# Kernel tuning notes

Hardware: AMD Instinct MI355X
Metric: run time of the kernel (lower is better)

Reference implementation:

```python
import jax, jax.numpy as jnp
import numpy as np
import math

B, T, V, D, H, L = 32, 512, 16, 256, 4, 2

def _ln(x, g, b, eps=1e-5):
    m = jnp.mean(x, -1, keepdims=True)
    v = jnp.mean((x - m) ** 2, -1, keepdims=True)
    return (x - m) * jax.lax.rsqrt(v + eps) * g + b

def _grn(x, w1, b1, w2, b2, g, bn, sw=None, sb=None):
    h = jax.nn.elu(x @ w1 + b1)
    h = h @ w2 + b2
    h1, h2 = jnp.split(h, 2, axis=-1)
    h = h1 * jax.nn.sigmoid(h2)
    skip = x if sw is None else x @ sw + sb
    return _ln(h + skip, g, bn)

def setup_inputs():
    ks = iter(jax.random.split(jax.random.key(0), 64))
    s = 0.02
    def w(*shape):
        return jax.random.normal(next(ks), shape, jnp.float32) * s
    return dict(
        x=jax.random.normal(next(ks), (B, T, V), jnp.float32),
        emb_w=w(V, D), emb_b=w(V, D),
        vg_fc1_w=w(V, D, D), vg_fc1_b=w(V, D), vg_fc2_w=w(V, D, 2 * D), vg_fc2_b=w(V, 2 * D),
        vg_ln_g=jnp.ones((V, D), jnp.float32), vg_ln_b=jnp.zeros((V, D), jnp.float32),
        sel_fc1_w=w(V * D, D), sel_fc1_b=w(D), sel_fc2_w=w(D, 2 * V), sel_fc2_b=w(2 * V),
        sel_skip_w=w(V * D, V), sel_skip_b=w(V),
        sel_ln_g=jnp.ones((V,), jnp.float32), sel_ln_b=jnp.zeros((V,), jnp.float32),
        lstm_wih=w(L, 4 * D, D), lstm_whh=w(L, 4 * D, D), lstm_bih=w(L, 4 * D), lstm_bhh=w(L, 4 * D),
        pl_fc1_w=w(D, D), pl_fc1_b=w(D), pl_fc2_w=w(D, 2 * D), pl_fc2_b=w(2 * D),
        pl_ln_g=jnp.ones((D,), jnp.float32), pl_ln_b=jnp.zeros((D,), jnp.float32),
        attn_in_w=w(3 * D, D), attn_in_b=w(3 * D), attn_out_w=w(D, D), attn_out_b=w(D),
        attn_ln_g=jnp.ones((D,), jnp.float32), attn_ln_b=jnp.zeros((D,), jnp.float32),
        pa_fc1_w=w(D, D), pa_fc1_b=w(D), pa_fc2_w=w(D, 2 * D), pa_fc2_b=w(2 * D),
        pa_ln_g=jnp.ones((D,), jnp.float32), pa_ln_b=jnp.zeros((D,), jnp.float32),
        fg_fc1_w=w(D, 4 * D), fg_fc1_b=w(4 * D), fg_fc2_w=w(4 * D, 2 * D), fg_fc2_b=w(2 * D),
        fg_ln_g=jnp.ones((D,), jnp.float32), fg_ln_b=jnp.zeros((D,), jnp.float32),
    )

def reference(x, emb_w, emb_b, vg_fc1_w, vg_fc1_b, vg_fc2_w, vg_fc2_b, vg_ln_g, vg_ln_b,
              sel_fc1_w, sel_fc1_b, sel_fc2_w, sel_fc2_b, sel_skip_w, sel_skip_b, sel_ln_g, sel_ln_b,
              lstm_wih, lstm_whh, lstm_bih, lstm_bhh,
              pl_fc1_w, pl_fc1_b, pl_fc2_w, pl_fc2_b, pl_ln_g, pl_ln_b,
              attn_in_w, attn_in_b, attn_out_w, attn_out_b, attn_ln_g, attn_ln_b,
              pa_fc1_w, pa_fc1_b, pa_fc2_w, pa_fc2_b, pa_ln_g, pa_ln_b,
              fg_fc1_w, fg_fc1_b, fg_fc2_w, fg_fc2_b, fg_ln_g, fg_ln_b):
    b, t, v = x.shape
    d = emb_w.shape[1]
    # per-feature Linear(1, d) fused into one broadcasted op: [B,T,V,D]
    embedded = x[..., None] * emb_w + emb_b
    # per-variable GRNs (no skip_fc since input==output), batched over V via einsum
    h = jax.nn.elu(jnp.einsum('btvd,vdh->btvh', embedded, vg_fc1_w) + vg_fc1_b)
    h = jnp.einsum('btvh,vho->btvo', h, vg_fc2_w) + vg_fc2_b
    h1, h2 = jnp.split(h, 2, axis=-1)
    var_out = _ln(h1 * jax.nn.sigmoid(h2) + embedded, vg_ln_g, vg_ln_b)  # [B,T,V,D]
    # selection GRN over flattened variables
    flat = embedded.reshape(b, t, v * d)
    sel = _grn(flat, sel_fc1_w, sel_fc1_b, sel_fc2_w, sel_fc2_b, sel_ln_g, sel_ln_b, sel_skip_w, sel_skip_b)
    weights = jax.nn.softmax(sel, axis=-1)  # [B,T,V]
    vsn_out = jnp.einsum('btvh,btv->bth', var_out, weights)  # [B,T,D]
    # stacked LSTM (torch gate order i,f,g,o); dropout inactive at eval
    h_seq = vsn_out
    for l in range(lstm_wih.shape[0]):
        xi = jnp.einsum('btd,gd->btg', h_seq, lstm_wih[l]) + lstm_bih[l] + lstm_bhh[l]
        whh = lstm_whh[l]
        def step(carry, xt):
            hp, cp = carry
            gates = xt + hp @ whh.T
            i, f, g, o = jnp.split(gates, 4, axis=-1)
            c = jax.nn.sigmoid(f) * cp + jax.nn.sigmoid(i) * jnp.tanh(g)
            hh = jax.nn.sigmoid(o) * jnp.tanh(c)
            return (hh, c), hh
        init = (jnp.zeros((b, d), x.dtype), jnp.zeros((b, d), x.dtype))
        _, hs = jax.lax.scan(step, init, jnp.swapaxes(xi, 0, 1))
        h_seq = jnp.swapaxes(hs, 0, 1)
    lstm_filtered = _grn(h_seq + vsn_out, pl_fc1_w, pl_fc1_b, pl_fc2_w, pl_fc2_b, pl_ln_g, pl_ln_b)
    # multihead self-attention
    qkv = lstm_filtered @ attn_in_w.T + attn_in_b
    q, k, vv = jnp.split(qkv, 3, axis=-1)
    hd = d // H
    def heads(z):
        return z.reshape(b, t, H, hd).transpose(0, 2, 1, 3)
    q, k, vv = heads(q), heads(k), heads(vv)
    scale = 1.0 / math.sqrt(hd)
    att = jax.nn.softmax(jnp.einsum('bhqd,bhkd->bhqk', q, k) * scale, axis=-1)
    o = jnp.einsum('bhqk,bhkd->bhqd', att, vv).transpose(0, 2, 1, 3).reshape(b, t, d)
    o = o @ attn_out_w.T + attn_out_b
    attn_out = _ln(o + lstm_filtered, attn_ln_g, attn_ln_b)
    attn_filtered = _grn(attn_out, pa_fc1_w, pa_fc1_b, pa_fc2_w, pa_fc2_b, pa_ln_g, pa_ln_b)
    out = _grn(attn_filtered, fg_fc1_w, fg_fc1_b, fg_fc2_w, fg_fc2_b, fg_ln_g, fg_ln_b)
    return out[:, -1, :], weights
```

## Files before the change

### kernel.cpp

```cpp
#include <hip/hip_runtime.h>
#include <hip/hip_bf16.h>
#include <hip/hip_fp8.h>
#include <math.h>


#define BT 16384
#define TT 512
#define BB 32
#define VV 16
#define DD 256

typedef unsigned short ushort;
typedef unsigned int uint;
typedef unsigned long ulong_;
typedef __attribute__((ext_vector_type(8))) short short8;
typedef __attribute__((ext_vector_type(8))) unsigned short ushort8v;
typedef __attribute__((ext_vector_type(4))) float floatx4;
typedef __attribute__((ext_vector_type(8))) int int8v;

#if __has_builtin(__builtin_amdgcn_cvt_pk_fp8_f32)
#define HW_FP8_CVT 1
#endif

__device__ __forceinline__ float sigmoidf_(float x) { return 1.f / (1.f + expf(-x)); }
__device__ __forceinline__ float eluf_(float x)     { return x > 0.f ? x : expm1f(x); }
__device__ __forceinline__ float fsig(float x) {
  return __builtin_amdgcn_rcpf(1.f + __expf(-x));
}
__device__ __forceinline__ float ftanh(float x) {
  float xc = fminf(fmaxf(x, -44.f), 44.f);
  float e = __expf(-2.f * xc);
  return (1.f - e) * __builtin_amdgcn_rcpf(1.f + e);
}
__device__ __forceinline__ ushort f2bf(float f) {
  unsigned int u = __float_as_uint(f);
  unsigned int r = u + 0x7fffu + ((u >> 16) & 1u);
  return (ushort)(r >> 16);
}
__device__ __forceinline__ float bf2f(ushort b) { return __uint_as_float(((unsigned int)b) << 16); }

__device__ __forceinline__ float2 bsum256x2(float a, float b, float* red8) {
  #pragma unroll
  for (int m = 32; m > 0; m >>= 1) { a += __shfl_xor(a, m, 64); b += __shfl_xor(b, m, 64); }
  int w = threadIdx.x >> 6;
  if ((threadIdx.x & 63) == 0) { red8[w * 2] = a; red8[w * 2 + 1] = b; }
  __syncthreads();
  float ra = red8[0] + red8[2] + red8[4] + red8[6];
  float rb = red8[1] + red8[3] + red8[5] + red8[7];
  __syncthreads();
  return make_float2(ra, rb);
}

__device__ __forceinline__ float block_sum256(float v, float* red) {
  int j = threadIdx.x;
  red[j] = v; __syncthreads();
  #pragma unroll
  for (int st = 128; st > 0; st >>= 1) {
    if (j < st) red[j] += red[j + st];
    __syncthreads();
  }
  float r = red[0];
  __syncthreads();
  return r;
}

__global__ void wtT_k(const float* __restrict__ src, ushort* __restrict__ dst,
                      int K, int N, long sStride, long dStride) {
  int b = blockIdx.z;
  src += (size_t)b * sStride; dst += (size_t)b * dStride;
  __shared__ float t[32][33];
  int k0 = blockIdx.y * 32, n0 = blockIdx.x * 32;
  int tx = threadIdx.x & 31, ty = threadIdx.x >> 5;
  #pragma unroll
  for (int i = 0; i < 32; i += 8) {
    int k = k0 + ty + i, n = n0 + tx;
    t[ty + i][tx] = (k < K && n < N) ? src[(size_t)k * N + n] : 0.f;
  }
  __syncthreads();
  #pragma unroll
  for (int i = 0; i < 32; i += 8) {
    int n = n0 + ty + i, k = k0 + tx;
    if (n < N && k < K) dst[(size_t)n * K + k] = f2bf(t[tx][ty + i]);
  }
}

__global__ void cvt_k(const float* __restrict__ src, ushort* __restrict__ dst, int n) {
  int i = blockIdx.x * 256 + threadIdx.x;
  if (i < n) dst[i] = f2bf(src[i]);
}

__global__ void whh_pack8_k(const float* __restrict__ whh, unsigned char* __restrict__ dst) {
  int gid = blockIdx.x * 256 + threadIdx.x;
  int layer = gid >> 13;
  int rem = gid & 8191;
  int lane = rem & 63;
  int f = (rem >> 6) & 15;
  int wave = rem >> 10;
  int kt2 = f & 1, ts = (f >> 1) & 1, g = f >> 2;
  int n = g * 256 + wave * 32 + ts * 16 + (lane & 15);
  int k0 = kt2 * 128 + (lane >> 4) * 32;
  const float* src = whh + (size_t)layer * 262144 + (size_t)n * 256 + k0;
  unsigned char* d = dst + (size_t)gid * 32;
  #pragma unroll
  for (int b = 0; b < 32; b++) {
    __hip_fp8_e4m3 q(src[b] * 64.f);
    d[b] = q.__x;
  }
}

template<int ADT, int ACT, int CDT>
__global__ __launch_bounds__(256) void mgemm_k(
    const void* __restrict__ Aall, int lda, long aStride,
    const ushort* __restrict__ Ball, long bStride,
    const float* __restrict__ biasAll, long biasStride,
    void* __restrict__ Call, int ldc, long cStride,
    int K, int Nvalid,
    const float* __restrict__ embw, const float* __restrict__ embb, int xbase) {
  int z = blockIdx.z;
  const ushort* B = Ball + (size_t)z * bStride;
  const float* bias = biasAll ? biasAll + (size_t)z * biasStride : nullptr;
  int m0 = blockIdx.y * 128, n0 = blockIdx.x * 128;
  __shared__ ushort As[128][40];
  __shared__ ushort Bs[128][40];
  int tid = threadIdx.x;
  int r = tid >> 1, half = tid & 1;
  int wave = tid >> 6, lane = tid & 63;
  int wm = (wave >> 1) * 64, wn = (wave & 1) * 64;
  int lm = lane & 15, lq = lane >> 4;
  floatx4 acc[4][4];
  #pragma unroll
  for (int i = 0; i < 4; i++)
    #pragma unroll
    for (int j = 0; j < 4; j++) acc[i][j] = (floatx4)0.f;

  for (int k0 = 0; k0 < K; k0 += 32) {
    int kk = k0 + half * 16;
    {
      int gm = m0 + r;
      ushort tmp[16];
      if (ADT == 0) {
        const float* Af = (const float*)Aall + (size_t)z * aStride + (size_t)gm * lda + kk;
        #pragma unroll
        for (int q = 0; q < 4; q++) {
          float4 f = ((const float4*)Af)[q];
          tmp[q * 4 + 0] = f2bf(f.x); tmp[q * 4 + 1] = f2bf(f.y);
          tmp[q * 4 + 2] = f2bf(f.z); tmp[q * 4 + 3] = f2bf(f.w);
        }
      } else if (ADT == 1) {
        const ushort* Ab = (const ushort*)Aall + (size_t)z * aStride + (size_t)gm * lda + kk;
        *(ushort8v*)&tmp[0] = *(const ushort8v*)(Ab);
        *(ushort8v*)&tmp[8] = *(const ushort8v*)(Ab + 8);
      } else if (ADT == 2) {
        const float* xp = (const float*)Aall;
        float xv = xp[(size_t)gm * lda + xbase + z + (kk >> 8)];
        const float4* ew = (const float4*)(embw + (size_t)z * 256 + kk);
        const float4* eb = (const float4*)(embb + (size_t)z * 256 + kk);
        #pragma unroll
        for (int q = 0; q < 4; q++) {
          float4 w4 = ew[q], b4 = eb[q];
          tmp[q * 4 + 0] = f2bf(xv * w4.x + b4.x); tmp[q * 4 + 1] = f2bf(xv * w4.y + b4.y);
          tmp[q * 4 + 2] = f2bf(xv * w4.z + b4.z); tmp[q * 4 + 3] = f2bf(xv * w4.w + b4.w);
        }
      } else {
        const float* A1 = (const float*)Aall + (size_t)z * aStride + (size_t)gm * lda + kk;
        const float* A2 = embw + (size_t)z * aStride + (size_t)gm * lda + kk;
        #pragma unroll
        for (int q = 0; q < 4; q++) {
          float4 f1 = ((const float4*)A1)[q];
          float4 f2 = ((const float4*)A2)[q];
          tmp[q * 4 + 0] = f2bf(f1.x + f2.x); tmp[q * 4 + 1] = f2bf(f1.y + f2.y);
          tmp[q * 4 + 2] = f2bf(f1.z + f2.z); tmp[q * 4 + 3] = f2bf(f1.w + f2.w);
        }
      }
      *(ushort8v*)&As[r][half * 16]     = *(ushort8v*)&tmp[0];
      *(ushort8v*)&As[r][half * 16 + 8] = *(ushort8v*)&tmp[8];
    }
    {
      int gn = n0 + r;
      ushort tmp[16];
      if (gn < Nvalid) {
        const ushort* Bp = B + (size_t)gn * K + kk;
        *(ushort8v*)&tmp[0] = *(const ushort8v*)(Bp);
        *(ushort8v*)&tmp[8] = *(const ushort8v*)(Bp + 8);
      } else {
        #pragma unroll
        for (int q = 0; q < 16; q++) tmp[q] = 0;
      }
      *(ushort8v*)&Bs[r][half * 16]     = *(ushort8v*)&tmp[0];
      *(ushort8v*)&Bs[r][half * 16 + 8] = *(ushort8v*)&tmp[8];
    }
    __syncthreads();
    short8 fa[4], fb[4];
    #pragma unroll
    for (int i = 0; i < 4; i++) fa[i] = *(const short8*)&As[wm + i * 16 + lm][lq * 8];
    #pragma unroll
    for (int j = 0; j < 4; j++) fb[j] = *(const short8*)&Bs[wn + j * 16 + lm][lq * 8];
    #pragma unroll
    for (int i = 0; i < 4; i++)
      #pragma unroll
      for (int j = 0; j < 4; j++)
        acc[i][j] = __builtin_amdgcn_mfma_f32_16x16x32_bf16(fa[i], fb[j], acc[i][j], 0, 0, 0);
    __syncthreads();
  }
  #pragma unroll
  for (int j = 0; j < 4; j++) {
    int gn = n0 + wn + j * 16 + lm;
    if (gn >= Nvalid) continue;
    float bv = bias ? bias[gn] : 0.f;
    #pragma unroll
    for (int i = 0; i < 4; i++) {
      #pragma unroll
      for (int rg = 0; rg < 4; rg++) {
        int gm = m0 + wm + i * 16 + lq * 4 + rg;
        float v = acc[i][j][rg] + bv;
        if (ACT == 1) v = eluf_(v);
        if (CDT == 0) ((float*)Call + (size_t)z * cStride)[(size_t)gm * ldc + gn] = v;
        else ((ushort*)Call + (size_t)z * cStride)[(size_t)gm * ldc + gn] = f2bf(v);
      }
    }
  }
}

__global__ void sel_finish_k(const float* __restrict__ selG, const float* __restrict__ selSkip,
                             const float* __restrict__ lng, const float* __restrict__ lnb,
                             float* __restrict__ wout, int M) {
  int m = blockIdx.x * 256 + threadIdx.x;
  if (m >= M) return;
  float s[16];
  float mean = 0.f;
  #pragma unroll
  for (int i = 0; i < 16; i++) {
    float h1 = selG[m * 32 + i], h2 = selG[m * 32 + 16 + i];
    float val = h1 * sigmoidf_(h2) + selSkip[m * 16 + i];
    s[i] = val; mean += val;
  }
  mean *= (1.f / 16.f);
  float var = 0.f;
  #pragma unroll
  for (int i = 0; i < 16; i++) { float d = s[i] - mean; var += d * d; }
  var *= (1.f / 16.f);
  float inv = rsqrtf(var + 1e-5f);
  float mx = -1e30f;
  #pragma unroll
  for (int i = 0; i < 16; i++) { s[i] = (s[i] - mean) * inv * lng[i] + lnb[i]; mx = fmaxf(mx, s[i]); }
  float sum = 0.f;
  #pragma unroll
  for (int i = 0; i < 16; i++) { s[i] = expf(s[i] - mx); sum += s[i]; }
  float isum = 1.f / sum;
  #pragma unroll
  for (int i = 0; i < 16; i++) wout[m * 16 + i] = s[i] * isum;
}

__global__ __launch_bounds__(256) void var_epi4_k(
    const ushort* __restrict__ G16,
    const float* __restrict__ x, int vbase,
    const float* __restrict__ embw, const float* __restrict__ embb,
    const float* __restrict__ lng, const float* __restrict__ lnb,
    const float* __restrict__ wts, float* __restrict__ vsn, int first) {
  int m = blockIdx.x, j = threadIdx.x;
  __shared__ float red8[8];
  float accv = 0.f;
  #pragma unroll
  for (int z = 0; z < 4; z++) {
    int v = vbase + z;
    const ushort* Gp = G16 + ((size_t)z * BT + m) * 512;
    float g1 = bf2f(Gp[j]), g2 = bf2f(Gp[256 + j]);
    float e = x[m * VV + v] * embw[z * 256 + j] + embb[z * 256 + j];
    float s = g1 * sigmoidf_(g2) + e;
    float2 r = bsum256x2(s, s * s, red8);
    float mean = r.x * (1.f / 256.f);
    float var = r.y * (1.f / 256.f) - mean * mean;
    float o = (s - mean) * rsqrtf(var + 1e-5f) * lng[z * 256 + j] + lnb[z * 256 + j];
    accv += wts[m * VV + v] * o;
  }
  size_t oi = (size_t)m * 256 + j;
  if (first) vsn[oi] = accv; else vsn[oi] += accv;
}

__global__ __launch_bounds__(256) void grn_epi_k(
    const ushort* __restrict__ G, const float* __restrict__ skipA,
    const float* __restrict__ skipB,
    const float* __restrict__ lng, const float* __restrict__ lnb,
    float* __restrict__ out) {
  int m = blockIdx.x, j = threadIdx.x;
  __shared__ float red8[8];
  float g1 = bf2f(G[(size_t)m * 512 + j]), g2 = bf2f(G[(size_t)m * 512 + 256 + j]);
  float sk = skipA[(size_t)m * 256 + j];
  if (skipB) sk += skipB[(size_t)m * 256 + j];
  float s = g1 * sigmoidf_(g2) + sk;
  float2 r = bsum256x2(s, s * s, red8);
  float mean = r.x * (1.f / 256.f);
  float var = r.y * (1.f / 256.f) - mean * mean;
  out[(size_t)m * 256 + j] = (s - mean) * rsqrtf(var + 1e-5f) * lng[j] + lnb[j];
}

__global__ void add2_k(const float* __restrict__ a, const float* __restrict__ b,
                       float* __restrict__ c, int n) {
  int i = blockIdx.x * 256 + threadIdx.x;
  if (i < n) c[i] = a[i] + b[i];
}

#define DESC (1.f / 1024.f)
#define H8S 272
__global__ __launch_bounds__(512, 2) void lstm_recur_k(
    const float* __restrict__ xi,
    const unsigned char* __restrict__ wpk,
    float* __restrict__ hout,
    int T) {
  int bb = blockIdx.x;
  int tid = threadIdx.x;
  int wave = tid >> 6, lane = tid & 63;
  int lm = lane & 15, lq = lane >> 4;
  __shared__ __align__(16) unsigned char h8[2][16 * H8S];
  for (int i = tid; i < 2 * 16 * H8S / 4; i += 512) ((uint*)h8)[i] = 0;

  int8v wr[16];
  {
    const int8v* wp = (const int8v*)wpk;
    #pragma unroll
    for (int f = 0; f < 16; f++) wr[f] = wp[(wave * 16 + f) * 64 + lane];
  }
  bool act = (lq == 0);
  int jj = wave * 32 + lm;
  const float* xg = xi + (size_t)bb * T * 1024;
  float xq[8], xn[8];
  if (act) {
    #pragma unroll
    for (int g = 0; g < 4; g++) {
      xq[2 * g]     = xg[g * 256 + jj];
      xq[2 * g + 1] = xg[g * 256 + jj + 16];
    }
  }
  float cst[2] = {0.f, 0.f};
  float hbf[2][8];
  int arow = lm * H8S + lq * 32;
  __syncthreads();

  for (int t = 0; t < T; t++) {
    int cur = t & 1, nxt = cur ^ 1;
    if (act && t + 1 < T) {
      const float* xp = xg + (size_t)(t + 1) * 1024;
      #pragma unroll
      for (int g = 0; g < 4; g++) {
        xn[2 * g]     = xp[g * 256 + jj];
        xn[2 * g + 1] = xp[g * 256 + jj + 16];
      }
    }
    int8v a[2];
    #pragma unroll
    for (int kt = 0; kt < 2; kt++)
      a[kt] = *(const int8v*)&h8[cur][arow + kt * 128];
    floatx4 acc[8];
    #pragma unroll
    for (int f = 0; f < 8; f++) acc[f] = (floatx4)0.f;
    #pragma unroll
    for (int kt = 0; kt < 2; kt++)
      #pragma unroll
      for (int f = 0; f < 8; f++)
        acc[f] = __builtin_amdgcn_mfma_scale_f32_16x16x128_f8f6f4(
            a[kt], wr[f * 2 + kt], acc[f], 0, 0, 0, 0x7f7f7f7f, 0, 0x7f7f7f7f);
    if (act) {
      int tb = t & 7;
      #pragma unroll
      for (int ts = 0; ts < 2; ts++) {
        float pi = acc[0 + ts][0] * DESC + xq[0 + ts];
        float pf = acc[2 + ts][0] * DESC + xq[2 + ts];
        float pg = acc[4 + ts][0] * DESC + xq[4 + ts];
        float po = acc[6 + ts][0] * DESC + xq[6 + ts];
        float c = fsig(pf) * cst[ts] + fsig(pi) * ftanh(pg);
        cst[ts] = c;
        hbf[ts][tb] = fsig(po) * ftanh(c);
      }
#ifdef HW_FP8_CVT
      int pk = __builtin_amdgcn_cvt_pk_fp8_f32(hbf[0][tb] * 16.f, hbf[1][tb] * 16.f, 0, false);
      h8[nxt][jj]      = (unsigned char)(pk & 0xff);
      h8[nxt][jj + 16] = (unsigned char)((pk >> 8) & 0xff);
#else
      __hip_fp8_e4m3 q0(hbf[0][tb] * 16.f), q1(hbf[1][tb] * 16.f);
      h8[nxt][jj]      = q0.__x;
      h8[nxt][jj + 16] = q1.__x;
#endif
      if (tb == 7) {
        #pragma unroll
        for (int q = 0; q < 8; q++) {
          size_t base = ((size_t)(bb * T + t - 7 + q)) * 256;
          hout[base + jj]      = hbf[0][q];
          hout[base + jj + 16] = hbf[1][q];
        }
      }
      #pragma unroll
      for (int g = 0; g < 8; g++) xq[g] = xn[g];
    }
    __syncthreads();
  }
}

__global__ __launch_bounds__(256) void attn_decode_k(const float* __restrict__ qkv,
                                                     float* __restrict__ o, int T) {
  int bh = blockIdx.x; int b = bh >> 2, h = bh & 3;
  int tid = threadIdx.x;
  __shared__ float q[64];
  __shared__ float p[512];
  __shared__ float red[256];
  if (tid < 64) q[tid] = qkv[((size_t)(b * T + T - 1)) * 768 + h * 64 + tid];
  __syncthreads();
  for (int t = tid; t < 512; t += 256) {
    const float* kv = qkv + ((size_t)(b * T + t)) * 768 + 256 + h * 64;
    float s = 0.f;
    #pragma unroll 16
    for (int d = 0; d < 64; d++) s += q[d] * kv[d];
    p[t] = s * 0.125f;
  }
  __syncthreads();
  red[tid] = fmaxf(p[tid], p[tid + 256]); __syncthreads();
  for (int st = 128; st > 0; st >>= 1) { if (tid < st) red[tid] = fmaxf(red[tid], red[tid + st]); __syncthreads(); }
  float mx = red[0]; __syncthreads();
  float e0 = expf(p[tid] - mx), e1 = expf(p[tid + 256] - mx);
  red[tid] = e0 + e1; __syncthreads();
  for (int st = 128; st > 0; st >>= 1) { if (tid < st) red[tid] += red[tid + st]; __syncthreads(); }
  float inv = 1.f / red[0];
  __syncthreads();
  p[tid] = e0; p[tid + 256] = e1;
  __syncthreads();
  int d = tid & 63, grp = tid >> 6;
  float acc = 0.f;
  for (int t = grp * 128; t < grp * 128 + 128; t++)
    acc += p[t] * qkv[((size_t)(b * T + t)) * 768 + 512 + h * 64 + d];
  red[tid] = acc; __syncthreads();
  if (grp == 0)
    o[(b * 4 + h) * 64 + d] = (red[tid] + red[tid + 64] + red[tid + 128] + red[tid + 192]) * inv;
}

__global__ __launch_bounds__(256) void attn_proj_ln_k(
    const float* __restrict__ attnO, const float* __restrict__ W, const float* __restrict__ bias,
    const float* __restrict__ lstmF, const float* __restrict__ lng, const float* __restrict__ lnb,
    float* __restrict__ out, int T) {
  int bb = blockIdx.x, j = threadIdx.x;
  __shared__ float a[256];
  __shared__ float red[256];
  a[j] = attnO[bb * 256 + j];
  __syncthreads();
  float acc = bias[j];
  const float* wr = W + (size_t)j * 256;
  #pragma unroll 8
  for (int k = 0; k < 256; k += 4) {
    float4 w4 = *(const float4*)(wr + k);
    acc += a[k] * w4.x + a[k + 1] * w4.y + a[k + 2] * w4.z + a[k + 3] * w4.w;
  }
  float s = acc + lstmF[((size_t)(bb * T + T - 1)) * 256 + j];
  float mean = block_sum256(s, red) * (1.f / 256.f);
  float d = s - mean;
  float var = block_sum256(d * d, red) * (1.f / 256.f);
  out[bb * 256 + j] = d * rsqrtf(var + 1e-5f) * lng[j] + lnb[j];
}

__global__ __launch_bounds__(256) void final_grns_k(
    const float* __restrict__ ain,
    const float* __restrict__ paw1, const float* __restrict__ pab1,
    const float* __restrict__ paw2, const float* __restrict__ pab2,
    const float* __restrict__ palg, const float* __restrict__ palb,
    const float* __restrict__ fgw1, const float* __restrict__ fgb1,
    const float* __restrict__ fgw2, const float* __restrict__ fgb2,
    const float* __restrict__ fglg, const float* __restrict__ fglb,
    float* __restrict__ out) {
  int bb = blockIdx.x, j = threadIdx.x;
  __shared__ float a[256];
  __shared__ float hbuf[1024];
  __shared__ float red[256];
  a[j] = ain[bb * 256 + j];
  __syncthreads();
  float acc = pab1[j];
  for (int k = 0; k < 256; k++) acc += a[k] * paw1[k * 256 + j];
  hbuf[j] = eluf_(acc);
  __syncthreads();
  float g1 = pab2[j], g2 = pab2[256 + j];
  for (int k = 0; k < 256; k++) { float hv = hbuf[k]; g1 += hv * paw2[k * 512 + j]; g2 += hv * paw2[k * 512 + 256 + j]; }
  float s = g1 * sigmoidf_(g2) + a[j];
  float mean = block_sum256(s, red) * (1.f / 256.f);
  float d = s - mean;
  float var = block_sum256(d * d, red) * (1.f / 256.f);
  float af = d * rsqrtf(var + 1e-5f) * palg[j] + palb[j];
  __syncthreads();
  a[j] = af;
  __syncthreads();
  float hh[4];
  #pragma unroll
  for (int q = 0; q < 4; q++) {
    int jj = j + q * 256;
    float ac = fgb1[jj];
    for (int k = 0; k < 256; k++) ac += a[k] * fgw1[k * 1024 + jj];
    hh[q] = eluf_(ac);
  }
  __syncthreads();
  #pragma unroll
  for (int q = 0; q < 4; q++) hbuf[j + q * 256] = hh[q];
  __syncthreads();
  float G1 = fgb2[j], G2 = fgb2[256 + j];
  for (int k = 0; k < 1024; k++) { float hv = hbuf[k]; G1 += hv * fgw2[k * 512 + j]; G2 += hv * fgw2[k * 512 + 256 + j]; }
  float s2 = G1 * sigmoidf_(G2) + a[j];
  mean = block_sum256(s2, red) * (1.f / 256.f);
  d = s2 - mean;
  var = block_sum256(d * d, red) * (1.f / 256.f);
  out[bb * 256 + j] = d * rsqrtf(var + 1e-5f) * fglg[j] + fglb[j];
}

extern "C" void kernel_launch(void* const* d_in, const int* in_sizes, int n_in,
                              void* d_out, int out_size, void* d_ws, size_t ws_size,
                              hipStream_t stream) {
  const float* x          = (const float*)d_in[0];
  const float* emb_w      = (const float*)d_in[1];
  const float* emb_b      = (const float*)d_in[2];
  const float* vg_fc1_w   = (const float*)d_in[3];
  const float* vg_fc1_b   = (const float*)d_in[4];
  const float* vg_fc2_w   = (const float*)d_in[5];
  const float* vg_fc2_b   = (const float*)d_in[6];
  const float* vg_ln_g    = (const float*)d_in[7];
  const float* vg_ln_b    = (const float*)d_in[8];
  const float* sel_fc1_w  = (const float*)d_in[9];
  const float* sel_fc1_b  = (const float*)d_in[10];
  const float* sel_fc2_w  = (const float*)d_in[11];
  const float* sel_fc2_b  = (const float*)d_in[12];
  const float* sel_skip_w = (const float*)d_in[13];
  const float* sel_skip_b = (const float*)d_in[14];
  const float* sel_ln_g   = (const float*)d_in[15];
  const float* sel_ln_b   = (const float*)d_in[16];
  const float* lstm_wih   = (const float*)d_in[17];
  const float* lstm_whh   = (const float*)d_in[18];
  const float* lstm_bih   = (const float*)d_in[19];
  const float* lstm_bhh   = (const float*)d_in[20];
  const float* pl_fc1_w   = (const float*)d_in[21];
  const float* pl_fc1_b   = (const float*)d_in[22];
  const float* pl_fc2_w   = (const float*)d_in[23];
  const float* pl_fc2_b   = (const float*)d_in[24];
  const float* pl_ln_g    = (const float*)d_in[25];
  const float* pl_ln_b    = (const float*)d_in[26];
  const float* attn_in_w  = (const float*)d_in[27];
  const float* attn_in_b  = (const float*)d_in[28];
  const float* attn_out_w = (const float*)d_in[29];
  const float* attn_out_b = (const float*)d_in[30];
  const float* attn_ln_g  = (const float*)d_in[31];
  const float* attn_ln_b  = (const float*)d_in[32];
  const float* pa_fc1_w   = (const float*)d_in[33];
  const float* pa_fc1_b   = (const float*)d_in[34];
  const float* pa_fc2_w   = (const float*)d_in[35];
  const float* pa_fc2_b   = (const float*)d_in[36];
  const float* pa_ln_g    = (const float*)d_in[37];
  const float* pa_ln_b    = (const float*)d_in[38];
  const float* fg_fc1_w   = (const float*)d_in[39];
  const float* fg_fc1_b   = (const float*)d_in[40];
  const float* fg_fc2_w   = (const float*)d_in[41];
  const float* fg_fc2_b   = (const float*)d_in[42];
  const float* fg_ln_g    = (const float*)d_in[43];
  const float* fg_ln_b    = (const float*)d_in[44];
  (void)in_sizes; (void)n_in; (void)out_size; (void)ws_size;

  float* out     = (float*)d_out;
  float* out_wts = out + BB * DD;

  char* p = (char*)d_ws;
  ushort* wt_sel_fc1  = (ushort*)p;                 p += 1048576 * 2;
  ushort* wt_sel_skip = (ushort*)p;                 p += 65536 * 2;
  ushort* wt_sel_fc2  = (ushort*)p;                 p += 8192 * 2;
  ushort* wt_var_fc1  = (ushort*)p;                 p += 1048576 * 2;
  ushort* wt_var_fc2  = (ushort*)p;                 p += 2097152 * 2;
  ushort* wt_wih      = (ushort*)p;                 p += 524288 * 2;
  unsigned char* wt_whh_pk8 = (unsigned char*)p;    p += 524288;
  ushort* wt_pl_fc1   = (ushort*)p;                 p += 65536 * 2;
  ushort* wt_pl_fc2   = (ushort*)p;                 p += 131072 * 2;
  ushort* wt_attn     = (ushort*)p;                 p += 196608 * 2;
  ushort* selH        = (ushort*)p;                 p += (size_t)BT * 256 * 2;
  float*  selSkip     = (float*)p;                  p += (size_t)BT * 16 * 4;
  float*  selG        = (float*)p;                  p += (size_t)BT * 32 * 4;
  float*  vsn         = (float*)p;                  p += (size_t)BT * 256 * 4;
  float*  hseq1       = (float*)p;                  p += (size_t)BT * 256 * 4;
  float*  hseq2       = (float*)p;                  p += (size_t)BT * 256 * 4;
  float*  cbias       = (float*)p;                  p += 4096 * 4;
  float*  attnO       = (float*)p;                  p += 8192 * 4;
  float*  attnLN      = (float*)p;                  p += 8192 * 4;
  char*   R           = p;
  ushort* bufA16 = (ushort*)R;
  ushort* bufG16 = (ushort*)(R + (((size_t)32) << 20));
  float*  xi     = (float*)R;
  ushort* plH    = (ushort*)(R + (((size_t)16) << 20));
  ushort* plG    = (ushort*)(R + (((size_t)24) << 20));
  float*  lstmF  = (float*)(R + (((size_t)48) << 20));
  float*  qkv    = (float*)R;

  dim3 blk(256);

  wtT_k<<<dim3(8, 128, 1),  blk, 0, stream>>>(sel_fc1_w,  wt_sel_fc1,  4096, 256, 0, 0);
  wtT_k<<<dim3(1, 128, 1),  blk, 0, stream>>>(sel_skip_w, wt_sel_skip, 4096, 16,  0, 0);
  wtT_k<<<dim3(1, 8, 1),    blk, 0, stream>>>(sel_fc2_w,  wt_sel_fc2,  256,  32,  0, 0);
  wtT_k<<<dim3(8, 8, 16),   blk, 0, stream>>>(vg_fc1_w,   wt_var_fc1,  256,  256, 65536, 65536);
  wtT_k<<<dim3(16, 8, 16),  blk, 0, stream>>>(vg_fc2_w,   wt_var_fc2,  256,  512, 131072, 131072);
  wtT_k<<<dim3(8, 8, 1),    blk, 0, stream>>>(pl_fc1_w,   wt_pl_fc1,   256,  256, 0, 0);
  wtT_k<<<dim3(16, 8, 1),   blk, 0, stream>>>(pl_fc2_w,   wt_pl_fc2,   256,  512, 0, 0);
  cvt_k<<<2048, blk, 0, stream>>>(lstm_wih,  wt_wih, 524288);
  whh_pack8_k<<<64, blk, 0, stream>>>(lstm_whh, wt_whh_pk8);
  cvt_k<<<768,  blk, 0, stream>>>(attn_in_w, wt_attn, 196608);
  add2_k<<<8, blk, 0, stream>>>(lstm_bih, lstm_bhh, cbias, 4096);

  mgemm_k<2,1,1><<<dim3(2, 128, 1), blk, 0, stream>>>(x, 16, 0, wt_sel_fc1, 0, sel_fc1_b, 0,
      selH, 256, 0, 4096, 256, emb_w, emb_b, 0);
  mgemm_k<2,0,0><<<dim3(1, 128, 1), blk, 0, stream>>>(x, 16, 0, wt_sel_skip, 0, sel_skip_b, 0,
      selSkip, 16, 0, 4096, 16, emb_w, emb_b, 0);
  mgemm_k<1,0,0><<<dim3(1, 128, 1), blk, 0, stream>>>(selH, 256, 0, wt_sel_fc2, 0, sel_fc2_b, 0,
      selG, 32, 0, 256, 32, nullptr, nullptr, 0);
  sel_finish_k<<<64, blk, 0, stream>>>(selG, selSkip, sel_ln_g, sel_ln_b, out_wts, BT);

  for (int g = 0; g < 4; g++) {
    mgemm_k<2,1,1><<<dim3(2, 128, 4), blk, 0, stream>>>(x, 16, 0,
        wt_var_fc1 + (size_t)g * 4 * 65536, 65536, vg_fc1_b + g * 1024, 256,
        bufA16, 256, (long)BT * 256, 256, 256, emb_w + g * 1024, emb_b + g * 1024, g * 4);
    mgemm_k<1,0,1><<<dim3(4, 128, 4), blk, 0, stream>>>(bufA16, 256, (long)BT * 256,
        wt_var_fc2 + (size_t)g * 4 * 131072, 131072, vg_fc2_b + g * 2048, 512,
        bufG16, 512, (long)BT * 512, 256, 512, nullptr, nullptr, 0);
    var_epi4_k<<<BT, blk, 0, stream>>>(bufG16, x, g * 4, emb_w + g * 1024, emb_b + g * 1024,
        vg_ln_g + g * 1024, vg_ln_b + g * 1024, out_wts, vsn, g == 0 ? 1 : 0);
  }

  mgemm_k<0,0,0><<<dim3(8, 128, 1), blk, 0, stream>>>(vsn, 256, 0, wt_wih, 0, cbias, 0,
      xi, 1024, 0, 256, 1024, nullptr, nullptr, 0);
  lstm_recur_k<<<32, 512, 0, stream>>>(xi, wt_whh_pk8, hseq1, TT);
  mgemm_k<0,0,0><<<dim3(8, 128, 1), blk, 0, stream>>>(hseq1, 256, 0, wt_wih + 1024 * 256, 0,
      cbias + 1024, 0, xi, 1024, 0, 256, 1024, nullptr, nullptr, 0);
  lstm_recur_k<<<32, 512, 0, stream>>>(xi, wt_whh_pk8 + 262144, hseq2, TT);

  mgemm_k<3,1,1><<<dim3(2, 128, 1), blk, 0, stream>>>(hseq2, 256, 0, wt_pl_fc1, 0, pl_fc1_b, 0,
      plH, 256, 0, 256, 256, vsn, nullptr, 0);
  mgemm_k<1,0,1><<<dim3(4, 128, 1), blk, 0, stream>>>(plH, 256, 0, wt_pl_fc2, 0, pl_fc2_b, 0,
      plG, 512, 0, 256, 512, nullptr, nullptr, 0);
  grn_epi_k<<<BT, blk, 0, stream>>>(plG, hseq2, vsn, pl_ln_g, pl_ln_b, lstmF);

  mgemm_k<0,0,0><<<dim3(6, 128, 1), blk, 0, stream>>>(lstmF, 256, 0, wt_attn, 0, attn_in_b, 0,
      qkv, 768, 0, 256, 768, nullptr, nullptr, 0);
  attn_decode_k<<<BB * 4, blk, 0, stream>>>(qkv, attnO, TT);
  attn_proj_ln_k<<<BB, blk, 0, stream>>>(attnO, attn_out_w, attn_out_b, lstmF,
                                         attn_ln_g, attn_ln_b, attnLN, TT);

  final_grns_k<<<BB, blk, 0, stream>>>(attnLN,
      pa_fc1_w, pa_fc1_b, pa_fc2_w, pa_fc2_b, pa_ln_g, pa_ln_b,
      fg_fc1_w, fg_fc1_b, fg_fc2_w, fg_fc2_b, fg_ln_g, fg_ln_b,
      out);
}
```

Baseline: 2.425 ms.

## Fold rank-1 embedding into first-layer weights, replacing K=4096 and K=256 GEMMs

Each embedded input is x*emb_w + emb_b, so the first linear layer of the selection GRN, its skip projection and each per-variable fc1 reduce to x*R + C. Small per-call kernels precompute R and C from the weights, and cheap elementwise kernels replace the large GEMMs, including the K=4096 selection GEMM. This removes the weight transposes and most of the FLOPs, at the cost of a serial 256-step reduction per weight column and fp32 accumulation order that differs from the original.

```diff
diff --git a/kernel.cpp b/kernel.cpp
--- a/kernel.cpp
+++ b/kernel.cpp
@@ -87,6 +87,68 @@
 __global__ void cvt_k(const float* __restrict__ src, ushort* __restrict__ dst, int n) {
   int i = blockIdx.x * 256 + threadIdx.x;
   if (i < n) dst[i] = f2bf(src[i]);
+}
+
+__global__ void redw_k(const float* __restrict__ W, int ldw,
+                       const float* __restrict__ ew, const float* __restrict__ eb,
+                       const float* __restrict__ bias, int biasPerV,
+                       float* __restrict__ R, float* __restrict__ C, int N) {
+  int v = blockIdx.x;
+  int n = threadIdx.x;
+  if (n >= N) return;
+  const float* Wb = W + (size_t)v * 256 * ldw + n;
+  const float* ewv = ew + v * 256;
+  const float* ebv = eb + v * 256;
+  float r = 0.f, c = 0.f;
+  for (int j = 0; j < 256; j++) {
+    float w = Wb[(size_t)j * ldw];
+    r += ewv[j] * w;
+    c += ebv[j] * w;
+  }
+  if (biasPerV) c += bias[v * 256 + n];
+  R[v * N + n] = r;
+  C[v * N + n] = c;
+}
+
+__global__ __launch_bounds__(256) void sel_h_k(const float* __restrict__ x,
+                                               const float* __restrict__ R1,
+                                               const float* __restrict__ C1,
+                                               const float* __restrict__ b1,
+                                               ushort* __restrict__ selH) {
+  int m = blockIdx.x, n = threadIdx.x;
+  __shared__ float xs[16];
+  if (n < 16) xs[n] = x[m * 16 + n];
+  __syncthreads();
+  float a = b1[n];
+  #pragma unroll
+  for (int v = 0; v < 16; v++) a += xs[v] * R1[v * 256 + n] + C1[v * 256 + n];
+  selH[(size_t)m * 256 + n] = f2bf(eluf_(a));
+}
+
+__global__ void sel_skip_k(const float* __restrict__ x,
+                           const float* __restrict__ Rsk, const float* __restrict__ Csk,
+                           const float* __restrict__ b, float* __restrict__ selSkip) {
+  int gid = blockIdx.x * 256 + threadIdx.x;
+  int m = gid >> 4, n = gid & 15;
+  const float* xr = x + m * 16;
+  float a = b[n];
+  #pragma unroll
+  for (int v = 0; v < 16; v++) a += xr[v] * Rsk[v * 16 + n] + Csk[v * 16 + n];
+  selSkip[gid] = a;
+}
+
+__global__ __launch_bounds__(256) void var_h_k(const float* __restrict__ x,
+                                               const float* __restrict__ R,
+                                               const float* __restrict__ C,
+                                               int vbase, ushort* __restrict__ bufA16) {
+  int m = blockIdx.x, n = threadIdx.x;
+  const float* xr = x + m * 16 + vbase;
+  #pragma unroll
+  for (int z = 0; z < 4; z++) {
+    int v = vbase + z;
+    float a = xr[z] * R[v * 256 + n] + C[v * 256 + n];
+    bufA16[((size_t)z * BT + m) * 256 + n] = f2bf(eluf_(a));
+  }
 }
 
 __global__ void whh_pack8_k(const float* __restrict__ whh, unsigned char* __restrict__ dst) {
@@ -558,16 +620,19 @@
   float* out_wts = out + BB * DD;
 
   char* p = (char*)d_ws;
-  ushort* wt_sel_fc1  = (ushort*)p;                 p += 1048576 * 2;
-  ushort* wt_sel_skip = (ushort*)p;                 p += 65536 * 2;
   ushort* wt_sel_fc2  = (ushort*)p;                 p += 8192 * 2;
-  ushort* wt_var_fc1  = (ushort*)p;                 p += 1048576 * 2;
   ushort* wt_var_fc2  = (ushort*)p;                 p += 2097152 * 2;
   ushort* wt_wih      = (ushort*)p;                 p += 524288 * 2;
   unsigned char* wt_whh_pk8 = (unsigned char*)p;    p += 524288;
   ushort* wt_pl_fc1   = (ushort*)p;                 p += 65536 * 2;
   ushort* wt_pl_fc2   = (ushort*)p;                 p += 131072 * 2;
   ushort* wt_attn     = (ushort*)p;                 p += 196608 * 2;
+  float*  selR        = (float*)p;                  p += 4096 * 4;
+  float*  selC        = (float*)p;                  p += 4096 * 4;
+  float*  varR        = (float*)p;                  p += 4096 * 4;
+  float*  varC        = (float*)p;                  p += 4096 * 4;
+  float*  skR         = (float*)p;                  p += 256 * 4;
+  float*  skC         = (float*)p;                  p += 256 * 4;
   ushort* selH        = (ushort*)p;                 p += (size_t)BT * 256 * 2;
   float*  selSkip     = (float*)p;                  p += (size_t)BT * 16 * 4;
   float*  selG        = (float*)p;                  p += (size_t)BT * 32 * 4;
@@ -588,10 +653,7 @@
 
   dim3 blk(256);
 
-  wtT_k<<<dim3(8, 128, 1),  blk, 0, stream>>>(sel_fc1_w,  wt_sel_fc1,  4096, 256, 0, 0);
-  wtT_k<<<dim3(1, 128, 1),  blk, 0, stream>>>(sel_skip_w, wt_sel_skip, 4096, 16,  0, 0);
   wtT_k<<<dim3(1, 8, 1),    blk, 0, stream>>>(sel_fc2_w,  wt_sel_fc2,  256,  32,  0, 0);
-  wtT_k<<<dim3(8, 8, 16),   blk, 0, stream>>>(vg_fc1_w,   wt_var_fc1,  256,  256, 65536, 65536);
   wtT_k<<<dim3(16, 8, 16),  blk, 0, stream>>>(vg_fc2_w,   wt_var_fc2,  256,  512, 131072, 131072);
   wtT_k<<<dim3(8, 8, 1),    blk, 0, stream>>>(pl_fc1_w,   wt_pl_fc1,   256,  256, 0, 0);
   wtT_k<<<dim3(16, 8, 1),   blk, 0, stream>>>(pl_fc2_w,   wt_pl_fc2,   256,  512, 0, 0);
@@ -599,19 +661,18 @@
   whh_pack8_k<<<64, blk, 0, stream>>>(lstm_whh, wt_whh_pk8);
   cvt_k<<<768,  blk, 0, stream>>>(attn_in_w, wt_attn, 196608);
   add2_k<<<8, blk, 0, stream>>>(lstm_bih, lstm_bhh, cbias, 4096);
-
-  mgemm_k<2,1,1><<<dim3(2, 128, 1), blk, 0, stream>>>(x, 16, 0, wt_sel_fc1, 0, sel_fc1_b, 0,
-      selH, 256, 0, 4096, 256, emb_w, emb_b, 0);
-  mgemm_k<2,0,0><<<dim3(1, 128, 1), blk, 0, stream>>>(x, 16, 0, wt_sel_skip, 0, sel_skip_b, 0,
-      selSkip, 16, 0, 4096, 16, emb_w, emb_b, 0);
+  redw_k<<<16, 256, 0, stream>>>(sel_fc1_w,  256, emb_w, emb_b, nullptr,   0, selR, selC, 256);
+  redw_k<<<16, 256, 0, stream>>>(vg_fc1_w,   256, emb_w, emb_b, vg_fc1_b,  1, varR, varC, 256);
+  redw_k<<<16, 64,  0, stream>>>(sel_skip_w, 16,  emb_w, emb_b, nullptr,   0, skR,  skC,  16);
+
+  sel_h_k<<<BT, blk, 0, stream>>>(x, selR, selC, sel_fc1_b, selH);
+  sel_skip_k<<<1024, blk, 0, stream>>>(x, skR, skC, sel_skip_b, selSkip);
   mgemm_k<1,0,0><<<dim3(1, 128, 1), blk, 0, stream>>>(selH, 256, 0, wt_sel_fc2, 0, sel_fc2_b, 0,
       selG, 32, 0, 256, 32, nullptr, nullptr, 0);
   sel_finish_k<<<64, blk, 0, stream>>>(selG, selSkip, sel_ln_g, sel_ln_b, out_wts, BT);
 
   for (int g = 0; g < 4; g++) {
-    mgemm_k<2,1,1><<<dim3(2, 128, 4), blk, 0, stream>>>(x, 16, 0,
-        wt_var_fc1 + (size_t)g * 4 * 65536, 65536, vg_fc1_b + g * 1024, 256,
-        bufA16, 256, (long)BT * 256, 256, 256, emb_w + g * 1024, emb_b + g * 1024, g * 4);
+    var_h_k<<<BT, blk, 0, stream>>>(x, varR, varC, g * 4, bufA16);
     mgemm_k<1,0,1><<<dim3(4, 128, 4), blk, 0, stream>>>(bufA16, 256, (long)BT * 256,
         wt_var_fc2 + (size_t)g * 4 * 131072, 131072, vg_fc2_b + g * 2048, 512,
         bufG16, 512, (long)BT * 512, 256, 512, nullptr, nullptr, 0);
```

New measurement: 2.168 ms. 1.12x faster.
